# Optimization experiments

Hardware: AMD Instinct MI355X
Metric: run time of the kernel (lower is better)

The kernel has to match this reference:

```python
import jax, jax.numpy as jnp
import numpy as np

N = 50000   # num nodes
E = 800000  # num edges (avg degree 16)
D = 64      # input feature dim
H = 64      # hidden dim
O = 32      # output dim


def setup_inputs() -> dict:
    key = jax.random.key(0)
    ks = jax.random.split(key, 8)
    def lin(k, fan_in, fan_out):
        # Kaiming-uniform-ish init, stored as [in, out] so forward is x @ W
        bound = 1.0 / np.sqrt(fan_in)
        return jax.random.uniform(k, (fan_in, fan_out), jnp.float32, -bound, bound)
    return {
        "x": jax.random.normal(ks[0], (N, D), jnp.float32),
        "edge_index": jax.random.randint(ks[1], (2, E), 0, N),
        "W_in1": lin(ks[2], D, H),
        "W_neigh1": lin(ks[3], D, H),
        "bias1": jnp.zeros((H,), jnp.float32),
        "W_in2": lin(ks[4], H, H),
        "W_neigh2": lin(ks[5], H, H),
        "bias2": jnp.zeros((H,), jnp.float32),
        "W_out": lin(ks[6], H, O),
        "b_out": jnp.zeros((O,), jnp.float32),
    }


def reference(x, edge_index, W_in1, W_neigh1, bias1, W_in2, W_neigh2, bias2, W_out, b_out):
    row, col = edge_index[0], edge_index[1]  # source, target
    # get_laplacian(sym) + remove_self_loops + negate -> norm = d^-1/2[row] * d^-1/2[col]
    deg = jax.ops.segment_sum(jnp.ones((E,), x.dtype), row, num_segments=N)
    dinv = jnp.where(deg > 0, deg ** -0.5, jnp.zeros((), x.dtype))
    norm = dinv[row] * dinv[col]  # [E]

    def conv(h, W_in, W_neigh, bias):
        # message: gather transformed source features, scale by per-edge norm
        msg = (h @ W_neigh)[row] * norm[:, None]          # [E, out]
        agg = jax.ops.segment_sum(msg, col, num_segments=N)  # scatter-add -> [N, out]
        return h @ W_in + agg + bias[None, :]

    h = jax.nn.relu(conv(x, W_in1, W_neigh1, bias1))
    h = jax.nn.relu(conv(h, W_in2, W_neigh2, bias2))
    return h @ W_out + b_out[None, :]  # variant='equi': per-node output [N, O]
```

## Files before the change

### kernel.cpp

```cpp
#include <hip/hip_runtime.h>
#include <hip/hip_bf16.h>


#define NCHUNK 32
#define NRANGE_B 4
#define HIST_B2 12544
#define SMEM1 100352

typedef __attribute__((ext_vector_type(8))) short bfrag;
typedef __attribute__((ext_vector_type(4))) float f32x4;

template <bool RELU, bool PRESCALE>
__device__ __forceinline__ void gemm_tile16(
    const float* h, const float* __restrict__ dinv,
    const short* Wn_f, const short* Wi_f, const float* b_s,
    __hip_bfloat16* __restrict__ t, float* agg, int r0, int lane, int N) {
  const int m = lane & 15;
  const int quad = lane >> 4;

  bfrag Bn[4][2], Bi[4][2];
#pragma unroll
  for (int ct = 0; ct < 4; ++ct)
#pragma unroll
    for (int kb = 0; kb < 2; ++kb) {
      Bn[ct][kb] = *(const bfrag*)&Wn_f[((ct * 2 + kb) * 64 + lane) * 8];
      Bi[ct][kb] = *(const bfrag*)&Wi_f[((ct * 2 + kb) * 64 + lane) * 8];
    }

  const int arow = r0 + m;
  bfrag A[2];
#pragma unroll
  for (int kb = 0; kb < 2; ++kb) {
    bfrag av = {};
    if (arow < N) {
      const float* src = &h[(size_t)arow * 64 + kb * 32 + quad * 8];
      float4 f0 = *(const float4*)src;
      float4 f1 = *(const float4*)(src + 4);
      float tmp[8] = {f0.x, f0.y, f0.z, f0.w, f1.x, f1.y, f1.z, f1.w};
#pragma unroll
      for (int j = 0; j < 8; ++j) {
        float v = RELU ? fmaxf(tmp[j], 0.f) : tmp[j];
        __hip_bfloat16 hb = __float2bfloat16(v);
        av[j] = *(short*)&hb;
      }
    }
    A[kb] = av;
  }

  f32x4 accT[4], accA[4];
#pragma unroll
  for (int ct = 0; ct < 4; ++ct) {
    f32x4 z = {0.f, 0.f, 0.f, 0.f};
    accT[ct] = z;
    accA[ct] = z;
  }
#pragma unroll
  for (int ct = 0; ct < 4; ++ct) {
    accT[ct] = __builtin_amdgcn_mfma_f32_16x16x32_bf16(A[0], Bn[ct][0], accT[ct], 0, 0, 0);
    accT[ct] = __builtin_amdgcn_mfma_f32_16x16x32_bf16(A[1], Bn[ct][1], accT[ct], 0, 0, 0);
    accA[ct] = __builtin_amdgcn_mfma_f32_16x16x32_bf16(A[0], Bi[ct][0], accA[ct], 0, 0, 0);
    accA[ct] = __builtin_amdgcn_mfma_f32_16x16x32_bf16(A[1], Bi[ct][1], accA[ct], 0, 0, 0);
  }

#pragma unroll
  for (int reg = 0; reg < 4; ++reg) {
    int r = r0 + quad * 4 + reg;
    if (r < N) {
      float dv = PRESCALE ? dinv[r] : 1.0f;
#pragma unroll
      for (int ct = 0; ct < 4; ++ct) {
        int col = ct * 16 + m;
        float tv = PRESCALE ? accT[ct][reg] * dv : accT[ct][reg];
        t[(size_t)r * 64 + col] = __float2bfloat16(tv);
        agg[(size_t)r * 64 + col] = accA[ct][reg] + b_s[col];
      }
    }
  }
}

__device__ __forceinline__ void stage_W_frag(const float* __restrict__ Wn,
                                             const float* __restrict__ Wi,
                                             short* Wn_f, short* Wi_f,
                                             int tid, int nthr) {
  for (int i = tid; i < 4096; i += nthr) {
    int k = i >> 6, n = i & 63;
    int dst = (((n >> 4) * 2 + (k >> 5)) * 64 + ((k >> 3) & 3) * 16 + (n & 15)) * 8 + (k & 7);
    __hip_bfloat16 a = __float2bfloat16(Wn[i]);
    __hip_bfloat16 b = __float2bfloat16(Wi[i]);
    Wn_f[dst] = *(short*)&a;
    Wi_f[dst] = *(short*)&b;
  }
}

__global__ __launch_bounds__(1024) void k_hist_gemm1(
    const int* __restrict__ ei, unsigned short* __restrict__ partial,
    const float* __restrict__ x,
    const float* __restrict__ Wn, const float* __restrict__ Wi,
    const float* __restrict__ bias,
    __hip_bfloat16* __restrict__ t, float* __restrict__ agg,
    int N, int E, int gemmBlocks) {
  __shared__ __align__(16) char smem[SMEM1];
  const int tid = threadIdx.x;

  if ((int)blockIdx.x < gemmBlocks) {
    short* Wn_f = (short*)smem;
    short* Wi_f = (short*)(smem + 8192);
    float* b_s = (float*)(smem + 16384);
    stage_W_frag(Wn, Wi, Wn_f, Wi_f, tid, 1024);
    if (tid < 64) b_s[tid] = bias[tid];
    __syncthreads();
    int w = tid >> 6;
    int lane = tid & 63;
    int r0 = blockIdx.x * 256 + w * 16;
    gemm_tile16<false, false>(x, nullptr, Wn_f, Wi_f, b_s, t, agg, r0, lane, N);
    return;
  }

  int* histw = (int*)smem;
  int bid = blockIdx.x - gemmBlocks;
  int c = bid % NCHUNK;
  int a = bid / NCHUNK;
  const int* ids = ei + (size_t)a * E;
  const int sw = (N + 1) & ~1;
  const int words = sw >> 1;
  for (int i = tid; i < words; i += 1024) histw[i] = 0;
  __syncthreads();
  int e0 = (int)((long long)E * c / NCHUNK);
  int e1 = (int)((long long)E * (c + 1) / NCHUNK);
  for (int e = e0 + tid; e < e1; e += 1024) {
    int s = ids[e];
    atomicAdd(&histw[s >> 1], 1 << ((s & 1) * 16));
  }
  __syncthreads();
  int* pdst = (int*)partial + (size_t)(a * NCHUNK + c) * words;
  for (int i = tid; i < words; i += 1024) pdst[i] = histw[i];
}

__global__ __launch_bounds__(256) void k_dinv_scan(const unsigned short* __restrict__ partial,
                                                   float* __restrict__ dinv,
                                                   int* __restrict__ indeg,
                                                   int* __restrict__ ptr,
                                                   int* __restrict__ bsum, int N) {
  __shared__ int s[256];
  const int sw = (N + 1) & ~1;
  int g = blockIdx.x * 256 + threadIdx.x;
  int deg = 0, ind = 0;
  if (g < N) {
#pragma unroll
    for (int c = 0; c < NCHUNK; ++c) {
      deg += partial[(size_t)c * sw + g];
      ind += partial[(size_t)(NCHUNK + c) * sw + g];
    }
    dinv[g] = (deg > 0) ? (1.0f / sqrtf((float)deg)) : 0.0f;
    indeg[g] = ind;
  }
  s[threadIdx.x] = ind;
  __syncthreads();
  for (int off = 1; off < 256; off <<= 1) {
    int tv = (threadIdx.x >= off) ? s[threadIdx.x - off] : 0;
    __syncthreads();
    s[threadIdx.x] += tv;
    __syncthreads();
  }
  if (g < N) ptr[g] = s[threadIdx.x] - ind;
  if (threadIdx.x == 255) bsum[blockIdx.x] = s[255];
}

__global__ __launch_bounds__(256) void k_base(const unsigned short* __restrict__ partial,
                                              const int* __restrict__ bsum,
                                              int* __restrict__ ptr,
                                              int* __restrict__ base, int N, int nb) {
  __shared__ int sb[256];
  const int sw = (N + 1) & ~1;
  int v = (threadIdx.x < nb) ? bsum[threadIdx.x] : 0;
  sb[threadIdx.x] = v;
  __syncthreads();
  for (int off = 1; off < 256; off <<= 1) {
    int tv = (threadIdx.x >= off) ? sb[threadIdx.x - off] : 0;
    __syncthreads();
    sb[threadIdx.x] += tv;
    __syncthreads();
  }
  __shared__ int pbs[256];
  pbs[threadIdx.x] = sb[threadIdx.x] - v;
  __syncthreads();
  int n = blockIdx.x * 256 + threadIdx.x;
  if (n >= N) return;
  int run = ptr[n] + pbs[n >> 8];
  ptr[n] = run;
#pragma unroll
  for (int c = 0; c < NCHUNK; ++c) {
    base[(size_t)c * N + n] = run;
    run += partial[(size_t)(NCHUNK + c) * sw + n];
  }
}

__global__ __launch_bounds__(1024) void k_bin2(const int* __restrict__ ei,
                                               const int* __restrict__ base,
                                               int* __restrict__ csr_row,
                                               int N, int E, int range) {
  __shared__ int cnt[HIST_B2];
  int c = blockIdx.x % NCHUNK;
  int r = blockIdx.x / NCHUNK;
  const int* row = ei;
  const int* col = ei + E;
  int lo = r * range;
  int hi = min(N, lo + range);
  int len = hi - lo;
  for (int i = threadIdx.x; i < len; i += 1024) cnt[i] = 0;
  __syncthreads();
  int e0 = (int)((long long)E * c / NCHUNK);
  int e1 = (int)((long long)E * (c + 1) / NCHUNK);
  const int* bslice = base + (size_t)c * N;
  for (int e = e0 + threadIdx.x; e < e1; e += 1024) {
    int cl = col[e];
    if (cl >= lo && cl < hi) {
      int rw = row[e];
      int off = atomicAdd(&cnt[cl - lo], 1);
      csr_row[bslice[cl] + off] = rw;
    }
  }
}

__global__ __launch_bounds__(1024) void k_gather_gemm2(
    const int* __restrict__ csr_row, const int* __restrict__ ptr,
    const int* __restrict__ indeg, const float* __restrict__ dinv,
    const __hip_bfloat16* __restrict__ t1, float* __restrict__ agg,
    const float* __restrict__ Wn, const float* __restrict__ Wi,
    const float* __restrict__ bias,
    __hip_bfloat16* __restrict__ t2, int N) {
  __shared__ short Wn_f[4096];
  __shared__ short Wi_f[4096];
  __shared__ float b_s[64];
  __shared__ float hrows[64 * 68];

  const int tid = threadIdx.x;
  stage_W_frag(Wn, Wi, Wn_f, Wi_f, tid, 1024);
  if (tid < 64) b_s[tid] = bias[tid];

  const int w = tid >> 6;
  const int lane = tid & 63;
  const int q = lane >> 4;
  const int fl = lane & 15;
  const int nn = w * 4 + q;
  const int base = (int)blockIdx.x * 64;
  const int n = base + nn;

  if (n < N) {
    int i0 = ptr[n];
    int end = i0 + indeg[n];
    float dn = dinv[n];
    float4 acc = make_float4(0.f, 0.f, 0.f, 0.f);
    int i = i0;
    for (; i + 1 < end; i += 2) {
      int ra = csr_row[i];
      int rb = csr_row[i + 1];
      float na = dinv[ra];
      float nb = dinv[rb];
      ushort4 ua = *(const ushort4*)&t1[(size_t)ra * 64 + 4 * fl];
      ushort4 ub = *(const ushort4*)&t1[(size_t)rb * 64 + 4 * fl];
      float4 va, vb;
      ((unsigned*)&va)[0] = (unsigned)ua.x << 16; ((unsigned*)&va)[1] = (unsigned)ua.y << 16;
      ((unsigned*)&va)[2] = (unsigned)ua.z << 16; ((unsigned*)&va)[3] = (unsigned)ua.w << 16;
      ((unsigned*)&vb)[0] = (unsigned)ub.x << 16; ((unsigned*)&vb)[1] = (unsigned)ub.y << 16;
      ((unsigned*)&vb)[2] = (unsigned)ub.z << 16; ((unsigned*)&vb)[3] = (unsigned)ub.w << 16;
      acc.x = fmaf(va.x, na, acc.x); acc.y = fmaf(va.y, na, acc.y);
      acc.z = fmaf(va.z, na, acc.z); acc.w = fmaf(va.w, na, acc.w);
      acc.x = fmaf(vb.x, nb, acc.x); acc.y = fmaf(vb.y, nb, acc.y);
      acc.z = fmaf(vb.z, nb, acc.z); acc.w = fmaf(vb.w, nb, acc.w);
    }
    if (i < end) {
      int ra = csr_row[i];
      float na = dinv[ra];
      ushort4 ua = *(const ushort4*)&t1[(size_t)ra * 64 + 4 * fl];
      float4 va;
      ((unsigned*)&va)[0] = (unsigned)ua.x << 16; ((unsigned*)&va)[1] = (unsigned)ua.y << 16;
      ((unsigned*)&va)[2] = (unsigned)ua.z << 16; ((unsigned*)&va)[3] = (unsigned)ua.w << 16;
      acc.x = fmaf(va.x, na, acc.x); acc.y = fmaf(va.y, na, acc.y);
      acc.z = fmaf(va.z, na, acc.z); acc.w = fmaf(va.w, na, acc.w);
    }
    float4 aggv = *(const float4*)&agg[(size_t)n * 64 + 4 * fl];
    f32x4 hv = {aggv.x + dn * acc.x, aggv.y + dn * acc.y,
                aggv.z + dn * acc.z, aggv.w + dn * acc.w};
    *(f32x4*)&hrows[nn * 68 + 4 * fl] = hv;
  } else {
    f32x4 z = {0.f, 0.f, 0.f, 0.f};
    *(f32x4*)&hrows[nn * 68 + 4 * fl] = z;
  }
  __syncthreads();

  if (w >= 4) return;
  const int m = fl;
  const int quad = q;

  bfrag Bn[4][2], Bi[4][2];
#pragma unroll
  for (int ct = 0; ct < 4; ++ct)
#pragma unroll
    for (int kb = 0; kb < 2; ++kb) {
      Bn[ct][kb] = *(const bfrag*)&Wn_f[((ct * 2 + kb) * 64 + lane) * 8];
      Bi[ct][kb] = *(const bfrag*)&Wi_f[((ct * 2 + kb) * 64 + lane) * 8];
    }

  bfrag A[2];
#pragma unroll
  for (int kb = 0; kb < 2; ++kb) {
    const float* src = &hrows[(w * 16 + m) * 68 + kb * 32 + quad * 8];
    float4 f0 = *(const float4*)src;
    float4 f1 = *(const float4*)(src + 4);
    float tmp[8] = {f0.x, f0.y, f0.z, f0.w, f1.x, f1.y, f1.z, f1.w};
    bfrag av;
#pragma unroll
    for (int j = 0; j < 8; ++j) {
      float v = fmaxf(tmp[j], 0.f);
      __hip_bfloat16 hb = __float2bfloat16(v);
      av[j] = *(short*)&hb;
    }
    A[kb] = av;
  }

  f32x4 accT[4], accA[4];
#pragma unroll
  for (int ct = 0; ct < 4; ++ct) {
    f32x4 z = {0.f, 0.f, 0.f, 0.f};
    accT[ct] = z;
    accA[ct] = z;
  }
#pragma unroll
  for (int ct = 0; ct < 4; ++ct) {
    accT[ct] = __builtin_amdgcn_mfma_f32_16x16x32_bf16(A[0], Bn[ct][0], accT[ct], 0, 0, 0);
    accT[ct] = __builtin_amdgcn_mfma_f32_16x16x32_bf16(A[1], Bn[ct][1], accT[ct], 0, 0, 0);
    accA[ct] = __builtin_amdgcn_mfma_f32_16x16x32_bf16(A[0], Bi[ct][0], accA[ct], 0, 0, 0);
    accA[ct] = __builtin_amdgcn_mfma_f32_16x16x32_bf16(A[1], Bi[ct][1], accA[ct], 0, 0, 0);
  }

#pragma unroll
  for (int reg = 0; reg < 4; ++reg) {
    int r = base + w * 16 + quad * 4 + reg;
    if (r < N) {
      float dv = dinv[r];
#pragma unroll
      for (int ct = 0; ct < 4; ++ct) {
        int col = ct * 16 + m;
        t2[(size_t)r * 64 + col] = __float2bfloat16(accT[ct][reg] * dv);
        agg[(size_t)r * 64 + col] = accA[ct][reg] + b_s[col];
      }
    }
  }
}

__global__ __launch_bounds__(256) void k_gather_out(
    const int* __restrict__ csr_row, const int* __restrict__ ptr,
    const int* __restrict__ indeg, const float* __restrict__ dinv,
    const __hip_bfloat16* __restrict__ t, const float* __restrict__ agg,
    const float* __restrict__ Wo,
    const float* __restrict__ bo,
    float* __restrict__ out, int N) {
  __shared__ float Wo_s[64 * 32];
  __shared__ float bo_s[32];
  __shared__ float rowbuf[4][64];

  const int tid = threadIdx.x;
  for (int i = tid; i < 2048; i += 256) Wo_s[i] = Wo[i];
  if (tid < 32) bo_s[tid] = bo[tid];
  __syncthreads();

  int w = tid >> 6;
  int n = blockIdx.x * 4 + w;
  if (n >= N) return;
  int lane = tid & 63;
  int q = lane >> 4;
  int fl = lane & 15;
  int i0 = ptr[n];
  int end = i0 + indeg[n];
  float dn = dinv[n];

  float4 aggv = make_float4(0.f, 0.f, 0.f, 0.f);
  if (q == 0) aggv = *(const float4*)&agg[(size_t)n * 64 + 4 * fl];

  float4 acc = make_float4(0.f, 0.f, 0.f, 0.f);
  int i = i0 + q;
  for (; i + 4 < end; i += 8) {
    int ra = csr_row[i];
    int rb = csr_row[i + 4];
    ushort4 ua = *(const ushort4*)&t[(size_t)ra * 64 + 4 * fl];
    ushort4 ub = *(const ushort4*)&t[(size_t)rb * 64 + 4 * fl];
    float4 va, vb;
    ((unsigned*)&va)[0] = (unsigned)ua.x << 16; ((unsigned*)&va)[1] = (unsigned)ua.y << 16;
    ((unsigned*)&va)[2] = (unsigned)ua.z << 16; ((unsigned*)&va)[3] = (unsigned)ua.w << 16;
    ((unsigned*)&vb)[0] = (unsigned)ub.x << 16; ((unsigned*)&vb)[1] = (unsigned)ub.y << 16;
    ((unsigned*)&vb)[2] = (unsigned)ub.z << 16; ((unsigned*)&vb)[3] = (unsigned)ub.w << 16;
    acc.x += va.x + vb.x; acc.y += va.y + vb.y;
    acc.z += va.z + vb.z; acc.w += va.w + vb.w;
  }
  for (; i < end; i += 4) {
    int ra = csr_row[i];
    ushort4 ua = *(const ushort4*)&t[(size_t)ra * 64 + 4 * fl];
    float4 va;
    ((unsigned*)&va)[0] = (unsigned)ua.x << 16; ((unsigned*)&va)[1] = (unsigned)ua.y << 16;
    ((unsigned*)&va)[2] = (unsigned)ua.z << 16; ((unsigned*)&va)[3] = (unsigned)ua.w << 16;
    acc.x += va.x; acc.y += va.y; acc.z += va.z; acc.w += va.w;
  }
  acc.x += __shfl_xor(acc.x, 16); acc.y += __shfl_xor(acc.y, 16);
  acc.z += __shfl_xor(acc.z, 16); acc.w += __shfl_xor(acc.w, 16);
  acc.x += __shfl_xor(acc.x, 32); acc.y += __shfl_xor(acc.y, 32);
  acc.z += __shfl_xor(acc.z, 32); acc.w += __shfl_xor(acc.w, 32);
  if (q == 0) {
    rowbuf[w][4 * fl + 0] = fmaxf(aggv.x + dn * acc.x, 0.f);
    rowbuf[w][4 * fl + 1] = fmaxf(aggv.y + dn * acc.y, 0.f);
    rowbuf[w][4 * fl + 2] = fmaxf(aggv.z + dn * acc.z, 0.f);
    rowbuf[w][4 * fl + 3] = fmaxf(aggv.w + dn * acc.w, 0.f);
  }
  int half = lane >> 5;
  int j = lane & 31;
  float ov = 0.f;
#pragma unroll 8
  for (int k = 32 * half; k < 32 * half + 32; ++k)
    ov = fmaf(rowbuf[w][k], Wo_s[k * 32 + j], ov);
  ov += __shfl_xor(ov, 32);
  if (half == 0) out[(size_t)n * 32 + j] = ov + bo_s[j];
}

extern "C" void kernel_launch(void* const* d_in, const int* in_sizes, int n_in,
                              void* d_out, int out_size, void* d_ws, size_t ws_size,
                              hipStream_t stream) {
  const float* x = (const float*)d_in[0];
  const int* ei = (const int*)d_in[1];
  const float* W_in1 = (const float*)d_in[2];
  const float* W_neigh1 = (const float*)d_in[3];
  const float* bias1 = (const float*)d_in[4];
  const float* W_in2 = (const float*)d_in[5];
  const float* W_neigh2 = (const float*)d_in[6];
  const float* bias2 = (const float*)d_in[7];
  const float* W_out = (const float*)d_in[8];
  const float* b_out = (const float*)d_in[9];
  float* out = (float*)d_out;

  const int N = in_sizes[0] / 64;
  const int E = in_sizes[1] / 2;

  char* ws = (char*)d_ws;
  size_t off = 0;
  auto alloc = [&](size_t bytes) -> void* {
    void* p = ws + off;
    off += (bytes + 255) & ~(size_t)255;
    return p;
  };
  const int sw = (N + 1) & ~1;
  float* dinv = (float*)alloc((size_t)N * 4);
  int* indeg = (int*)alloc((size_t)N * 4);
  int* ptr = (int*)alloc((size_t)N * 4);
  int* bsum = (int*)alloc(1024);
  int* csr_row = (int*)alloc((size_t)E * 4);
  unsigned short* partial = (unsigned short*)alloc((size_t)2 * NCHUNK * sw * 2);
  int* base = (int*)alloc((size_t)NCHUNK * N * 4);
  __hip_bfloat16* t = (__hip_bfloat16*)alloc((size_t)N * 64 * 2);
  __hip_bfloat16* t2 = (__hip_bfloat16*)alloc((size_t)N * 64 * 2);
  float* agg = (float*)alloc((size_t)N * 64 * 4);
  (void)ws_size;

  int range_b = (N + NRANGE_B - 1) / NRANGE_B;
  int gN = (N + 255) / 256;
  int gNode = (N + 3) / 4;
  int gFused = (N + 63) / 64;
  int nb = (N + 255) / 256;
  int gemmBlocks = (N + 255) / 256;

  k_hist_gemm1<<<gemmBlocks + 2 * NCHUNK, 1024, 0, stream>>>(
      ei, partial, x, W_neigh1, W_in1, bias1, t, agg, N, E, gemmBlocks);
  k_dinv_scan<<<nb, 256, 0, stream>>>(partial, dinv, indeg, ptr, bsum, N);
  k_base<<<gN, 256, 0, stream>>>(partial, bsum, ptr, base, N, nb);
  k_bin2<<<NRANGE_B * NCHUNK, 1024, 0, stream>>>(ei, base, csr_row, N, E, range_b);

  k_gather_gemm2<<<gFused, 1024, 0, stream>>>(csr_row, ptr, indeg, dinv, t, agg,
                                              W_neigh2, W_in2, bias2, t2, N);

  k_gather_out<<<gNode, 256, 0, stream>>>(csr_row, ptr, indeg, dinv, t2, agg,
                                          W_out, b_out, out, N);
}
```

Before: 190.2 us.

## Merge degree scan, base computation and CSR binning into one persistent kernel

Replaces three launches (dinv/scan, block-sum base, binning) with a single 128-block kernel that uses a software grid barrier built on global atomic counters to separate the phases. The barrier counters are reset by the preceding histogram kernel. This removes two kernel launch gaps and their drain/fill costs. In exchange it relies on all 128 blocks being co-resident, which is assumed rather than guaranteed, and it uses fewer, larger scan blocks.

```diff
diff --git a/kernel.cpp b/kernel.cpp
--- a/kernel.cpp
+++ b/kernel.cpp
@@ -6,9 +6,27 @@
 #define NRANGE_B 4
 #define HIST_B2 12544
 #define SMEM1 100352
+#define NB_BUILD (NRANGE_B * NCHUNK)
 
 typedef __attribute__((ext_vector_type(8))) short bfrag;
 typedef __attribute__((ext_vector_type(4))) float f32x4;
+
+__device__ __forceinline__ void gsync(int* cnt, int* gen, int nb) {
+  __syncthreads();
+  if (threadIdx.x == 0) {
+    int my = atomicAdd(gen, 0);
+    __threadfence();
+    int prev = atomicAdd(cnt, 1);
+    if (prev == nb * (my + 1) - 1) {
+      __threadfence();
+      atomicAdd(gen, 1);
+    } else {
+      while (atomicAdd(gen, 0) == my) __builtin_amdgcn_s_sleep(2);
+      __threadfence();
+    }
+  }
+  __syncthreads();
+}
 
 template <bool RELU, bool PRESCALE>
 __device__ __forceinline__ void gemm_tile16(
@@ -98,6 +116,7 @@
     const float* __restrict__ Wn, const float* __restrict__ Wi,
     const float* __restrict__ bias,
     __hip_bfloat16* __restrict__ t, float* __restrict__ agg,
+    int* __restrict__ bars,
     int N, int E, int gemmBlocks) {
   __shared__ __align__(16) char smem[SMEM1];
   const int tid = threadIdx.x;
@@ -118,6 +137,7 @@
 
   int* histw = (int*)smem;
   int bid = blockIdx.x - gemmBlocks;
+  if (bid == 0 && tid < 4) bars[tid] = 0;
   int c = bid % NCHUNK;
   int a = bid / NCHUNK;
   const int* ids = ei + (size_t)a * E;
@@ -136,16 +156,25 @@
   for (int i = tid; i < words; i += 1024) pdst[i] = histw[i];
 }
 
-__global__ __launch_bounds__(256) void k_dinv_scan(const unsigned short* __restrict__ partial,
-                                                   float* __restrict__ dinv,
-                                                   int* __restrict__ indeg,
-                                                   int* __restrict__ ptr,
-                                                   int* __restrict__ bsum, int N) {
-  __shared__ int s[256];
+__global__ __launch_bounds__(1024) void k_build(
+    const int* __restrict__ ei,
+    const unsigned short* __restrict__ partial,
+    float* __restrict__ dinv, int* __restrict__ indeg,
+    int* __restrict__ ptr, int* __restrict__ base,
+    int* __restrict__ csr_row, int* __restrict__ bsum,
+    int* __restrict__ bars,
+    int N, int E, int range_b) {
+  __shared__ int smem[HIST_B2];
+  const int tid = threadIdx.x;
+  const int b = blockIdx.x;
+  const int nbB = NB_BUILD;
   const int sw = (N + 1) & ~1;
-  int g = blockIdx.x * 256 + threadIdx.x;
-  int deg = 0, ind = 0;
-  if (g < N) {
+  const int npb = (N + nbB - 1) / nbB;
+  const int g = b * npb + tid;
+
+  int ind = 0;
+  if (tid < npb && g < N) {
+    int deg = 0;
 #pragma unroll
     for (int c = 0; c < NCHUNK; ++c) {
       deg += partial[(size_t)c * sw + g];
@@ -154,69 +183,57 @@
     dinv[g] = (deg > 0) ? (1.0f / sqrtf((float)deg)) : 0.0f;
     indeg[g] = ind;
   }
-  s[threadIdx.x] = ind;
-  __syncthreads();
-  for (int off = 1; off < 256; off <<= 1) {
-    int tv = (threadIdx.x >= off) ? s[threadIdx.x - off] : 0;
+  smem[tid] = ind;
+  __syncthreads();
+  for (int off = 1; off < 1024; off <<= 1) {
+    int tv = (tid >= off) ? smem[tid - off] : 0;
     __syncthreads();
-    s[threadIdx.x] += tv;
+    smem[tid] += tv;
     __syncthreads();
   }
-  if (g < N) ptr[g] = s[threadIdx.x] - ind;
-  if (threadIdx.x == 255) bsum[blockIdx.x] = s[255];
-}
-
-__global__ __launch_bounds__(256) void k_base(const unsigned short* __restrict__ partial,
-                                              const int* __restrict__ bsum,
-                                              int* __restrict__ ptr,
-                                              int* __restrict__ base, int N, int nb) {
-  __shared__ int sb[256];
-  const int sw = (N + 1) & ~1;
-  int v = (threadIdx.x < nb) ? bsum[threadIdx.x] : 0;
-  sb[threadIdx.x] = v;
-  __syncthreads();
-  for (int off = 1; off < 256; off <<= 1) {
-    int tv = (threadIdx.x >= off) ? sb[threadIdx.x - off] : 0;
+  const int ex = smem[tid] - ind;
+  if (tid == 0) bsum[b] = smem[1023];
+
+  gsync(&bars[0], &bars[1], nbB);
+
+  smem[tid] = (tid < nbB) ? bsum[tid] : 0;
+  __syncthreads();
+  for (int off = 1; off < 1024; off <<= 1) {
+    int tv = (tid >= off) ? smem[tid - off] : 0;
     __syncthreads();
-    sb[threadIdx.x] += tv;
+    smem[tid] += tv;
     __syncthreads();
   }
-  __shared__ int pbs[256];
-  pbs[threadIdx.x] = sb[threadIdx.x] - v;
-  __syncthreads();
-  int n = blockIdx.x * 256 + threadIdx.x;
-  if (n >= N) return;
-  int run = ptr[n] + pbs[n >> 8];
-  ptr[n] = run;
-#pragma unroll
-  for (int c = 0; c < NCHUNK; ++c) {
-    base[(size_t)c * N + n] = run;
-    run += partial[(size_t)(NCHUNK + c) * sw + n];
-  }
-}
-
-__global__ __launch_bounds__(1024) void k_bin2(const int* __restrict__ ei,
-                                               const int* __restrict__ base,
-                                               int* __restrict__ csr_row,
-                                               int N, int E, int range) {
-  __shared__ int cnt[HIST_B2];
-  int c = blockIdx.x % NCHUNK;
-  int r = blockIdx.x / NCHUNK;
+  const int pb = (b == 0) ? 0 : smem[b - 1];
+  if (tid < npb && g < N) {
+    int run = ex + pb;
+    ptr[g] = run;
+#pragma unroll
+    for (int c = 0; c < NCHUNK; ++c) {
+      base[(size_t)c * N + g] = run;
+      run += partial[(size_t)(NCHUNK + c) * sw + g];
+    }
+  }
+
+  gsync(&bars[0], &bars[1], nbB);
+
+  int c = b % NCHUNK;
+  int r = b / NCHUNK;
   const int* row = ei;
   const int* col = ei + E;
-  int lo = r * range;
-  int hi = min(N, lo + range);
+  int lo = r * range_b;
+  int hi = min(N, lo + range_b);
   int len = hi - lo;
-  for (int i = threadIdx.x; i < len; i += 1024) cnt[i] = 0;
+  for (int i = tid; i < len; i += 1024) smem[i] = 0;
   __syncthreads();
   int e0 = (int)((long long)E * c / NCHUNK);
   int e1 = (int)((long long)E * (c + 1) / NCHUNK);
   const int* bslice = base + (size_t)c * N;
-  for (int e = e0 + threadIdx.x; e < e1; e += 1024) {
+  for (int e = e0 + tid; e < e1; e += 1024) {
     int cl = col[e];
     if (cl >= lo && cl < hi) {
       int rw = row[e];
-      int off = atomicAdd(&cnt[cl - lo], 1);
+      int off = atomicAdd(&smem[cl - lo], 1);
       csr_row[bslice[cl] + off] = rw;
     }
   }
@@ -451,6 +468,7 @@
   int* indeg = (int*)alloc((size_t)N * 4);
   int* ptr = (int*)alloc((size_t)N * 4);
   int* bsum = (int*)alloc(1024);
+  int* bars = (int*)alloc(256);
   int* csr_row = (int*)alloc((size_t)E * 4);
   unsigned short* partial = (unsigned short*)alloc((size_t)2 * NCHUNK * sw * 2);
   int* base = (int*)alloc((size_t)NCHUNK * N * 4);
@@ -460,17 +478,15 @@
   (void)ws_size;
 
   int range_b = (N + NRANGE_B - 1) / NRANGE_B;
-  int gN = (N + 255) / 256;
   int gNode = (N + 3) / 4;
   int gFused = (N + 63) / 64;
-  int nb = (N + 255) / 256;
   int gemmBlocks = (N + 255) / 256;
 
   k_hist_gemm1<<<gemmBlocks + 2 * NCHUNK, 1024, 0, stream>>>(
-      ei, partial, x, W_neigh1, W_in1, bias1, t, agg, N, E, gemmBlocks);
-  k_dinv_scan<<<nb, 256, 0, stream>>>(partial, dinv, indeg, ptr, bsum, N);
-  k_base<<<gN, 256, 0, stream>>>(partial, bsum, ptr, base, N, nb);
-  k_bin2<<<NRANGE_B * NCHUNK, 1024, 0, stream>>>(ei, base, csr_row, N, E, range_b);
+      ei, partial, x, W_neigh1, W_in1, bias1, t, agg, bars, N, E, gemmBlocks);
+
+  k_build<<<NB_BUILD, 1024, 0, stream>>>(ei, partial, dinv, indeg, ptr, base,
+                                         csr_row, bsum, bars, N, E, range_b);
 
   k_gather_gemm2<<<gFused, 1024, 0, stream>>>(csr_row, ptr, indeg, dinv, t, agg,
                                               W_neigh2, W_in2, bias2, t2, N);
```

After: 211.3 us. 11.1% more time.
